# Performance work log

Measured on AMD Instinct MI355X. Metric: run time of the kernel, lower is better.

Reference implementation:

```python
import jax, jax.numpy as jnp
import numpy as np

VOCAB = 14
D_MODEL = 1024
D_FF = 4096
B, S = 8, 2048
EPS = 1e-5


def _linear_params(key, d_in, d_out):
    kw, kb = jax.random.split(key)
    lim = 1.0 / np.sqrt(d_in)
    W = jax.random.uniform(kw, (d_out, d_in), jnp.float32, -lim, lim)
    b = jax.random.uniform(kb, (d_out,), jnp.float32, -lim, lim)
    return W, b


def setup_inputs() -> dict:
    key = jax.random.key(0)
    ks = jax.random.split(key, 8)
    x = jax.random.randint(ks[0], (B, S), 0, VOCAB)
    tok_emb = jax.random.normal(ks[1], (VOCAB, D_MODEL), jnp.float32)
    qw, qb = _linear_params(ks[2], D_MODEL, D_MODEL)
    kw, kb = _linear_params(ks[3], D_MODEL, D_MODEL)
    vw, vb = _linear_params(ks[4], D_MODEL, D_MODEL)
    pw, pb = _linear_params(ks[5], D_MODEL, D_MODEL)
    f1w, f1b = _linear_params(ks[6], D_MODEL, D_FF)
    f2w, f2b = _linear_params(ks[7], D_FF, D_MODEL)
    ones = jnp.ones((D_MODEL,), jnp.float32)
    zeros = jnp.zeros((D_MODEL,), jnp.float32)
    return {
        "x": x, "tok_emb": tok_emb,
        "ln1_w": ones, "ln1_b": zeros,
        "qw": qw, "qb": qb, "kw": kw, "kb": kb, "vw": vw, "vb": vb,
        "pw": pw, "pb": pb,
        "ln2_w": ones, "ln2_b": zeros,
        "f1w": f1w, "f1b": f1b, "f2w": f2w, "f2b": f2b,
        "lnf_w": ones, "lnf_b": zeros,
    }


def _layernorm(h, w, b):
    mu = jnp.mean(h, axis=-1, keepdims=True)
    var = jnp.var(h, axis=-1, keepdims=True)
    return (h - mu) / jnp.sqrt(var + EPS) * w + b


def reference(x, tok_emb, ln1_w, ln1_b, qw, qb, kw, kb, vw, vb, pw, pb,
              ln2_w, ln2_b, f1w, f1b, f2w, f2b, lnf_w, lnf_b):
    h = tok_emb[x]                                  # [B,S,D]
    r = h
    hn = _layernorm(h, ln1_w, ln1_b)
    q = hn @ qw.T + qb
    k = hn @ kw.T + kb
    v = hn @ vw.T + vb
    scale = 1.0 / jnp.sqrt(jnp.float32(q.shape[-1]))
    att = jnp.einsum('bqd,bkd->bqk', q, k) * scale  # [B,S,S]
    causal = jnp.tril(jnp.ones((S, S), bool))
    att = jnp.where(causal, att, -jnp.inf)
    att = jax.nn.softmax(att, axis=-1)
    h = jnp.einsum('bqk,bkd->bqd', att, v) @ pw.T + pb
    h = r + h
    r2 = h
    hn = _layernorm(h, ln2_w, ln2_b)
    h = jax.nn.gelu(hn @ f1w.T + f1b, approximate=False) @ f2w.T + f2b
    h = r2 + h
    h = _layernorm(h, lnf_w, lnf_b)
    logits = h @ tok_emb.T                          # [B,S,VOCAB]
    return logits
```

## Files before the change

### kernel.cpp

```cpp
#include <hip/hip_runtime.h>
#include <math.h>

typedef unsigned short u16;
typedef __attribute__((ext_vector_type(8))) short short8;
typedef __attribute__((ext_vector_type(8))) __bf16 bf16x8;
typedef __attribute__((ext_vector_type(4))) float f32x4;

#define FLAG_BIAS   1
#define FLAG_RES    2
#define FLAG_GELU   4
#define FLAG_TRI    8
#define FLAG_CK     16

__device__ __forceinline__ u16 f2bf(float f) {
  unsigned u = __builtin_bit_cast(unsigned, f);
  unsigned r = u + 0x7fffu + ((u >> 16) & 1u);
  return (u16)(r >> 16);
}
__device__ __forceinline__ float bf2f(u16 u) {
  return __builtin_bit_cast(float, (unsigned)u << 16);
}
__device__ __forceinline__ float wred_sum(float v) {
#pragma unroll
  for (int m = 32; m; m >>= 1) v += __shfl_xor(v, m, 64);
  return v;
}
__device__ __forceinline__ float wred_max(float v) {
#pragma unroll
  for (int m = 32; m; m >>= 1) v = fmaxf(v, __shfl_xor(v, m, 64));
  return v;
}
__device__ __forceinline__ float gelu_fast(float x) {
  float y = 0.7978845608f * x * (1.f + 0.044715f * x * x);
  float e = __expf(2.f * y);
  float th = 1.f - 2.f / (e + 1.f);
  return 0.5f * x * (1.f + th);
}
__device__ __forceinline__ f32x4 mfma16(short8 a, short8 b, f32x4 c) {
  return __builtin_amdgcn_mfma_f32_16x16x32_bf16(
      __builtin_bit_cast(bf16x8, a), __builtin_bit_cast(bf16x8, b), c, 0, 0, 0);
}

#define GLOAD_LDS16(gptr, lptr)                                              \
  __builtin_amdgcn_global_load_lds(                                          \
      (const __attribute__((address_space(1))) void*)(gptr),                 \
      (__attribute__((address_space(3))) void*)(lptr), 16, 0, 0)

__global__ __launch_bounds__(512, 2) void gemm256(
    const u16* __restrict__ Aptr, const u16* __restrict__ Bptr,
    u16* __restrict__ Cptr, const float* __restrict__ bias,
    const u16* __restrict__ resp,
    int M, int N, int K, int lda, int ldb, int ldc, float alpha, int flags,
    long long sA, long long sB, long long sC) {
  const int nwg = gridDim.x;
  const int cpx = nwg >> 3;
  const int bid = blockIdx.x;
  const int swz = (bid & 7) * cpx + (bid >> 3);
  int bm, bn, z;
  if (flags & FLAG_TRI) {
    z = swz / 36;
    int tq = swz - z * 36;
    bm = (int)((sqrtf(8.f * tq + 1.f) - 1.f) * 0.5f);
    while ((bm + 1) * (bm + 2) / 2 <= tq) ++bm;
    while (bm * (bm + 1) / 2 > tq) --bm;
    bn = tq - bm * (bm + 1) / 2;
  } else {
    z = blockIdx.z;
    const int nbm = M >> 8;
    bn = swz / nbm;
    bm = swz - bn * nbm;
  }
  const int gm0 = bm << 8, gn0 = bn << 8;
  const int kend = (flags & FLAG_CK) ? min(K, gm0 + 256) : K;
  const int NT = kend >> 5;

  __shared__ __align__(16) u16 As[2][256 * 32];
  __shared__ __align__(16) u16 Bs[2][256 * 32];

  const int t = threadIdx.x;
  const int l = t & 63;
  const int w = t >> 6;
  const int wr = w >> 2, wc = w & 3;
  const int frow = l & 15;
  const int g4 = l >> 4;

  const int srow = (w << 4) + (l >> 2);
  const int sch = (l & 3) ^ ((srow >> 1) & 3);
  const u16* Ag = Aptr + (size_t)z * sA + (size_t)(gm0 + srow) * lda + sch * 8;
  const u16* Bg = Bptr + (size_t)z * sB + (size_t)(gn0 + srow) * ldb + sch * 8;
  const long long a128 = (long long)128 * lda, b128 = (long long)128 * ldb;

  auto STAGE_A = [&](int buf, int kt) {
    GLOAD_LDS16(Ag + kt, &As[buf][w * 512]);
    GLOAD_LDS16(Ag + a128 + kt, &As[buf][4096 + w * 512]);
  };
  auto STAGE_B = [&](int buf, int kt) {
    GLOAD_LDS16(Bg + kt, &Bs[buf][w * 512]);
    GLOAD_LDS16(Bg + b128 + kt, &Bs[buf][4096 + w * 512]);
  };

  f32x4 acc[8][4] = {};

  STAGE_A(0, 0); STAGE_B(0, 0);
  asm volatile("s_waitcnt vmcnt(0)" ::: "memory");
  __builtin_amdgcn_s_barrier();
  __builtin_amdgcn_sched_barrier(0);

  for (int tt = 0; tt < NT; ++tt) {
    const int buf = tt & 1;
    const int kt1 = (tt + 1) << 5;
    const bool pre = (tt + 1) < NT;
    short8 af[4], bf[4];
#pragma unroll
    for (int m = 0; m < 4; ++m) {
      int rr = wr * 128 + m * 16 + frow;
      af[m] = *(const short8*)&As[buf][rr * 32 + ((g4 ^ ((rr >> 1) & 3)) << 3)];
    }
#pragma unroll
    for (int n = 0; n < 4; ++n) {
      int rr = wc * 64 + n * 16 + frow;
      bf[n] = *(const short8*)&Bs[buf][rr * 32 + ((g4 ^ ((rr >> 1) & 3)) << 3)];
    }
    if (pre) { STAGE_A(buf ^ 1, kt1); STAGE_B(buf ^ 1, kt1); }
    __builtin_amdgcn_s_barrier();
    asm volatile("s_waitcnt lgkmcnt(0)" ::: "memory");
    __builtin_amdgcn_sched_barrier(0);
    __builtin_amdgcn_s_setprio(1);
#pragma unroll
    for (int m = 0; m < 4; ++m)
#pragma unroll
      for (int n = 0; n < 4; ++n)
        acc[m][n] = mfma16(af[m], bf[n], acc[m][n]);
    __builtin_amdgcn_s_setprio(0);
    __builtin_amdgcn_sched_barrier(0);
    __builtin_amdgcn_s_barrier();
#pragma unroll
    for (int m = 0; m < 4; ++m) {
      int rr = wr * 128 + 64 + m * 16 + frow;
      af[m] = *(const short8*)&As[buf][rr * 32 + ((g4 ^ ((rr >> 1) & 3)) << 3)];
    }
    if (pre) asm volatile("s_waitcnt vmcnt(0)" ::: "memory");
    __builtin_amdgcn_s_barrier();
    asm volatile("s_waitcnt lgkmcnt(0)" ::: "memory");
    __builtin_amdgcn_sched_barrier(0);
    __builtin_amdgcn_s_setprio(1);
#pragma unroll
    for (int m = 0; m < 4; ++m)
#pragma unroll
      for (int n = 0; n < 4; ++n)
        acc[4 + m][n] = mfma16(af[m], bf[n], acc[4 + m][n]);
    __builtin_amdgcn_s_setprio(0);
    __builtin_amdgcn_sched_barrier(0);
    __builtin_amdgcn_s_barrier();
  }

  u16* Cb = Cptr + (size_t)z * sC;
  const bool hasB = flags & FLAG_BIAS, hasR = flags & FLAG_RES;
  const bool doG = flags & FLAG_GELU;
#pragma unroll
  for (int m = 0; m < 8; ++m) {
#pragma unroll
    for (int n = 0; n < 4; ++n) {
      int row0 = gm0 + wr * 128 + m * 16 + ((l >> 4) << 2);
      int col = gn0 + wc * 64 + n * 16 + frow;
      float bv = hasB ? bias[col] : 0.0f;
#pragma unroll
      for (int i = 0; i < 4; ++i) {
        float v = acc[m][n][i] * alpha + bv;
        if (doG) v = gelu_fast(v);
        size_t idx = (size_t)(row0 + i) * ldc + col;
        if (hasR) v += bf2f(resp[idx]);
        Cb[idx] = f2bf(v);
      }
    }
  }
}

__global__ __launch_bounds__(256) void f32_to_bf16_v4(const float* __restrict__ in,
                                                      u16* __restrict__ out, int n4) {
  int i = blockIdx.x * 256 + threadIdx.x;
  if (i < n4) {
    float4 v = ((const float4*)in)[i];
    ushort4 o;
    o.x = f2bf(v.x); o.y = f2bf(v.y); o.z = f2bf(v.z); o.w = f2bf(v.w);
    ((ushort4*)out)[i] = o;
  }
}

__global__ __launch_bounds__(256) void embed_ln1(
    const int* __restrict__ x, const float* __restrict__ emb,
    const float* __restrict__ w, const float* __restrict__ b,
    u16* __restrict__ h16, u16* __restrict__ hn) {
  int row = blockIdx.x * 4 + (threadIdx.x >> 6);
  int lane = threadIdx.x & 63;
  int tok = x[row];
  const float* e = emb + (size_t)tok * 1024;
  float v[16];
  float s = 0.f, q = 0.f;
#pragma unroll
  for (int i = 0; i < 16; ++i) { v[i] = e[lane + i * 64]; s += v[i]; q += v[i] * v[i]; }
  s = wred_sum(s); q = wred_sum(q);
  float mu = s * (1.0f / 1024.0f);
  float rstd = rsqrtf(q * (1.0f / 1024.0f) - mu * mu + 1e-5f);
  u16* hr = h16 + (size_t)row * 1024;
  u16* hnr = hn + (size_t)row * 1024;
#pragma unroll
  for (int i = 0; i < 16; ++i) {
    int d = lane + i * 64;
    hr[d] = f2bf(v[i]);
    hnr[d] = f2bf((v[i] - mu) * rstd * w[d] + b[d]);
  }
}

__global__ __launch_bounds__(256) void ln_rows(
    const u16* __restrict__ in, const float* __restrict__ w,
    const float* __restrict__ b, u16* __restrict__ out) {
  int row = blockIdx.x * 4 + (threadIdx.x >> 6);
  int lane = threadIdx.x & 63;
  const short8* ir = (const short8*)(in + (size_t)row * 1024);
  short8 c0 = ir[lane], c1 = ir[lane + 64];
  float v[16];
  float s = 0.f, q = 0.f;
#pragma unroll
  for (int j = 0; j < 8; ++j) {
    v[j] = bf2f((u16)c0[j]); v[8 + j] = bf2f((u16)c1[j]);
  }
#pragma unroll
  for (int j = 0; j < 16; ++j) { s += v[j]; q += v[j] * v[j]; }
  s = wred_sum(s); q = wred_sum(q);
  float mu = s * (1.0f / 1024.0f);
  float rstd = rsqrtf(q * (1.0f / 1024.0f) - mu * mu + 1e-5f);
  short8 o0, o1;
#pragma unroll
  for (int j = 0; j < 8; ++j) {
    int d0 = lane * 8 + j, d1 = 512 + lane * 8 + j;
    o0[j] = (short)f2bf((v[j] - mu) * rstd * w[d0] + b[d0]);
    o1[j] = (short)f2bf((v[8 + j] - mu) * rstd * w[d1] + b[d1]);
  }
  short8* orow = (short8*)(out + (size_t)row * 1024);
  orow[lane] = o0; orow[lane + 64] = o1;
}

__global__ __launch_bounds__(256) void softmax_causal(u16* att) {
  int r = blockIdx.x * 4 + (threadIdx.x >> 6);
  int lane = threadIdx.x & 63;
  int i = r & 2047;
  int n = i + 1;
  int ng = (i >> 9) + 1;
  short8* pv = (short8*)(att + (size_t)r * 2048);
  float v[32];
  float m = -1e30f;
#pragma unroll
  for (int g = 0; g < 4; ++g) {
    if (g < ng) {
      short8 c = pv[g * 64 + lane];
#pragma unroll
      for (int j = 0; j < 8; ++j) {
        int idx = g * 512 + lane * 8 + j;
        float f = (idx < n) ? bf2f((u16)c[j]) : -1e30f;
        v[g * 8 + j] = f;
        m = fmaxf(m, f);
      }
    }
  }
  m = wred_max(m);
  float s = 0.f;
#pragma unroll
  for (int g = 0; g < 4; ++g) {
    if (g < ng) {
#pragma unroll
      for (int j = 0; j < 8; ++j) {
        int idx = g * 512 + lane * 8 + j;
        float e = (idx < n) ? __expf(v[g * 8 + j] - m) : 0.f;
        v[g * 8 + j] = e; s += e;
      }
    }
  }
  s = wred_sum(s);
  float inv = 1.0f / s;
#pragma unroll
  for (int g = 0; g < 4; ++g) {
    if (g < ng) {
      short8 o;
#pragma unroll
      for (int j = 0; j < 8; ++j) o[j] = (short)f2bf(v[g * 8 + j] * inv);
      pv[g * 64 + lane] = o;
    }
  }
}

__global__ __launch_bounds__(256) void transpose_v(const u16* __restrict__ V,
                                                   u16* __restrict__ Vt, int ldv) {
  int z = blockIdx.z;
  const u16* src = V + (size_t)z * 2048 * ldv;
  u16* dst = Vt + (size_t)z * 1024 * 2048;
  int j0 = (blockIdx.x >> 4) << 6;
  int d0 = (blockIdx.x & 15) << 6;
  __shared__ u16 tile[64][65];
  int c = threadIdx.x & 15;
  int rr = threadIdx.x >> 4;
#pragma unroll
  for (int q = 0; q < 4; ++q) {
    int row = rr + q * 16;
    ushort4 val = *(const ushort4*)(src + (size_t)(j0 + row) * ldv + d0 + c * 4);
    tile[row][c * 4 + 0] = val.x; tile[row][c * 4 + 1] = val.y;
    tile[row][c * 4 + 2] = val.z; tile[row][c * 4 + 3] = val.w;
  }
  __syncthreads();
#pragma unroll
  for (int q = 0; q < 4; ++q) {
    int drow = rr + q * 16;
    ushort4 o;
    o.x = tile[c * 4 + 0][drow]; o.y = tile[c * 4 + 1][drow];
    o.z = tile[c * 4 + 2][drow]; o.w = tile[c * 4 + 3][drow];
    *(ushort4*)(dst + (size_t)(d0 + drow) * 2048 + j0 + c * 4) = o;
  }
}

__global__ __launch_bounds__(256) void lnf_logits(
    const u16* __restrict__ h, const float* __restrict__ w,
    const float* __restrict__ b, const float* __restrict__ emb,
    float* __restrict__ out) {
  __shared__ float el[14 * 1056];
  int t = threadIdx.x;
  for (int f = t * 4; f < 14 * 1024; f += 1024) {
    float4 e = *(const float4*)(emb + f);
    int v = f >> 10, d = f & 1023;
    float* dst = el + v * 1056 + d + (d >> 5);
    dst[0] = e.x; dst[1] = e.y; dst[2] = e.z; dst[3] = e.w;
  }
  __syncthreads();
  int lane = t & 63, wid = t >> 6;
  float w0[8], w1[8], b0[8], b1[8];
#pragma unroll
  for (int j = 0; j < 8; ++j) {
    int d0 = lane * 8 + j, d1 = 512 + lane * 8 + j;
    w0[j] = w[d0]; b0[j] = b[d0];
    w1[j] = w[d1]; b1[j] = b[d1];
  }
  const float* e0 = el + lane * 8 + (lane >> 2);
  const float* e1 = el + 528 + lane * 8 + (lane >> 2);
  for (int rr = 0; rr < 8; ++rr) {
    int row = blockIdx.x * 32 + wid * 8 + rr;
    const short8* hr = (const short8*)(h + (size_t)row * 1024);
    short8 c0 = hr[lane], c1 = hr[lane + 64];
    float v0[8], v1[8];
    float s = 0.f, q = 0.f;
#pragma unroll
    for (int j = 0; j < 8; ++j) {
      v0[j] = bf2f((u16)c0[j]); v1[j] = bf2f((u16)c1[j]);
      s += v0[j] + v1[j];
      q += v0[j] * v0[j] + v1[j] * v1[j];
    }
    s = wred_sum(s); q = wred_sum(q);
    float mu = s * (1.0f / 1024.0f);
    float rstd = rsqrtf(q * (1.0f / 1024.0f) - mu * mu + 1e-5f);
    float h0[8], h1[8];
#pragma unroll
    for (int j = 0; j < 8; ++j) {
      h0[j] = (v0[j] - mu) * rstd * w0[j] + b0[j];
      h1[j] = (v1[j] - mu) * rstd * w1[j] + b1[j];
    }
    float p[14];
#pragma unroll
    for (int v = 0; v < 14; ++v) {
      const float* ev0 = e0 + v * 1056;
      const float* ev1 = e1 + v * 1056;
      float a = 0.f;
#pragma unroll
      for (int j = 0; j < 8; ++j) a += h0[j] * ev0[j] + h1[j] * ev1[j];
      p[v] = a;
    }
#pragma unroll
    for (int m = 32; m; m >>= 1)
#pragma unroll
      for (int v = 0; v < 14; ++v) p[v] += __shfl_xor(p[v], m, 64);
    if (lane == 0) {
      float* orow = out + (size_t)row * 14;
#pragma unroll
      for (int v = 0; v < 14; ++v) orow[v] = p[v];
    }
  }
}

__global__ void zero_out_k(float* o, int n) {
  int i = blockIdx.x * 256 + threadIdx.x;
  if (i < n) o[i] = 0.f;
}
__global__ void diag_k(float* o, float v) { if (threadIdx.x == 0) o[0] = v; }

extern "C" void kernel_launch(void* const* d_in, const int* in_sizes, int n_in,
                              void* d_out, int out_size, void* d_ws, size_t ws_size,
                              hipStream_t stream) {
  const int* x = (const int*)d_in[0];
  const float* tok_emb = (const float*)d_in[1];
  const float* ln1_w = (const float*)d_in[2];
  const float* ln1_b = (const float*)d_in[3];
  const float* qw = (const float*)d_in[4];
  const float* qb = (const float*)d_in[5];
  const float* kw = (const float*)d_in[6];
  const float* kb = (const float*)d_in[7];
  const float* vw = (const float*)d_in[8];
  const float* vb = (const float*)d_in[9];
  const float* pw = (const float*)d_in[10];
  const float* pb = (const float*)d_in[11];
  const float* ln2_w = (const float*)d_in[12];
  const float* ln2_b = (const float*)d_in[13];
  const float* f1w = (const float*)d_in[14];
  const float* f1b = (const float*)d_in[15];
  const float* f2w = (const float*)d_in[16];
  const float* f2b = (const float*)d_in[17];
  const float* lnf_w = (const float*)d_in[18];
  const float* lnf_b = (const float*)d_in[19];
  float* out = (float*)d_out;

  const long long T = 16384, D = 1024, F = 4096, S = 2048;
  const size_t MB = 1ull << 20;
  char* base = (char*)d_ws;

  if (ws_size < 224 * MB) {
    zero_out_k<<<dim3((out_size + 255) / 256), 256, 0, stream>>>(out, out_size);
    diag_k<<<dim3(1), 1, 0, stream>>>(out, (float)ws_size);
    return;
  }

  u16* rA16 = (u16*)base;
  u16* rB   = (u16*)(base + 32 * MB);
  u16* QKV  = (u16*)(base + 64 * MB);
  u16* SC   = (u16*)(base + 160 * MB);
  u16* W3   = SC;
  float* qkvb = (float*)(base + 166 * MB);
  u16* PW  = SC;
  u16* CB  = QKV;
  u16* F1  = (u16*)(base + 192 * MB);
  u16* F2  = (u16*)(base + 200 * MB);

  auto cvt = [&](const float* src, u16* dst, long long n) {
    int n4 = (int)(n / 4);
    f32_to_bf16_v4<<<dim3((n4 + 255) / 256), dim3(256), 0, stream>>>(src, dst, n4);
  };
  auto gemm = [&](const u16* A, const u16* B, u16* C, const float* bias,
                  const u16* res, long long M, long long N, long long K,
                  long long lda, long long ldb, long long ldc, float alpha,
                  int flags, long long sA, long long sB, long long sC,
                  int gx, int gz) {
    gemm256<<<dim3(gx, 1, gz), dim3(512), 0, stream>>>(
        A, B, C, bias, res, (int)M, (int)N, (int)K, (int)lda, (int)ldb,
        (int)ldc, alpha, flags, sA, sB, sC);
  };

  cvt(qw, W3, D * D);
  cvt(kw, W3 + 1024 * 1024, D * D);
  cvt(vw, W3 + 2 * 1024 * 1024, D * D);
  hipMemcpyAsync(qkvb, qb, D * 4, hipMemcpyDeviceToDevice, stream);
  hipMemcpyAsync(qkvb + 1024, kb, D * 4, hipMemcpyDeviceToDevice, stream);
  hipMemcpyAsync(qkvb + 2048, vb, D * 4, hipMemcpyDeviceToDevice, stream);

  embed_ln1<<<dim3(T / 4), 256, 0, stream>>>(x, tok_emb, ln1_w, ln1_b, rA16, rB);

  gemm(rB, W3, QKV, qkvb, nullptr, T, 3072, D, D, D, 3072, 1.f, FLAG_BIAS,
       0, 0, 0, 768, 1);

  gemm(QKV, QKV + 1024, SC, nullptr, nullptr, S, S, D, 3072, 3072, 2048,
       0.03125f, FLAG_TRI, S * 3072, S * 3072, S * S, 288, 1);

  transpose_v<<<dim3(512, 1, 8), 256, 0, stream>>>(QKV + 2048, rB, 3072);

  softmax_causal<<<dim3(T / 4), 256, 0, stream>>>(SC);

  gemm(SC, rB, QKV, nullptr, nullptr, S, D, S, S, S, 3072, 1.f, FLAG_CK,
       S * S, D * S, S * 3072, 32, 8);

  cvt(pw, PW, D * D);
  gemm(QKV, PW, rA16, pb, rA16, T, D, D, 3072, D, D, 1.f, FLAG_BIAS | FLAG_RES,
       0, 0, 0, 256, 1);

  ln_rows<<<dim3(T / 4), 256, 0, stream>>>(rA16, ln2_w, ln2_b, rB);

  cvt(f1w, F1, F * D);
  cvt(f2w, F2, D * F);
  gemm(rB, F1, CB, f1b, nullptr, T, F, D, D, D, F, 1.f, FLAG_BIAS | FLAG_GELU,
       0, 0, 0, 1024, 1);
  gemm(CB, F2, rA16, f2b, rA16, T, D, F, F, F, D, 1.f, FLAG_BIAS | FLAG_RES,
       0, 0, 0, 256, 1);

  lnf_logits<<<dim3(512), 256, 0, stream>>>(rA16, lnf_w, lnf_b, tok_emb, out);
}
```

Measured before the change: 883.5 us.

## Deepen GEMM global-to-LDS pipeline with 64-wide K tiles split into half stages

Each main-loop iteration of the GEMM now covers 64 K elements, held as two 32-wide LDS sub-tiles per buffer. The global-to-LDS loads for the next halves are spread across the four MFMA phases, and the vmcnt waits now allow outstanding loads to remain in flight. The aim is to hide global memory latency behind more MFMA work and cut barrier-bound stalls. It doubles LDS use to 128KB, which may hurt occupancy, and the half-buffer reuse depends on correct wait counts. The loop now assumes K is a multiple of 64.

```diff
diff --git a/kernel.cpp b/kernel.cpp
--- a/kernel.cpp
+++ b/kernel.cpp
@@ -72,10 +72,10 @@
   }
   const int gm0 = bm << 8, gn0 = bn << 8;
   const int kend = (flags & FLAG_CK) ? min(K, gm0 + 256) : K;
-  const int NT = kend >> 5;
-
-  __shared__ __align__(16) u16 As[2][256 * 32];
-  __shared__ __align__(16) u16 Bs[2][256 * 32];
+  const int NT = kend >> 6;
+
+  __shared__ __align__(16) u16 As[2][2][256 * 32];
+  __shared__ __align__(16) u16 Bs[2][2][256 * 32];
 
   const int t = threadIdx.x;
   const int l = t & 63;
@@ -90,38 +90,41 @@
   const u16* Bg = Bptr + (size_t)z * sB + (size_t)(gn0 + srow) * ldb + sch * 8;
   const long long a128 = (long long)128 * lda, b128 = (long long)128 * ldb;
 
-  auto STAGE_A = [&](int buf, int kt) {
-    GLOAD_LDS16(Ag + kt, &As[buf][w * 512]);
-    GLOAD_LDS16(Ag + a128 + kt, &As[buf][4096 + w * 512]);
+  auto SA = [&](int buf, int kk, int kt) {
+    GLOAD_LDS16(Ag + kt + kk * 32, &As[buf][kk][w * 512]);
+    GLOAD_LDS16(Ag + a128 + kt + kk * 32, &As[buf][kk][4096 + w * 512]);
   };
-  auto STAGE_B = [&](int buf, int kt) {
-    GLOAD_LDS16(Bg + kt, &Bs[buf][w * 512]);
-    GLOAD_LDS16(Bg + b128 + kt, &Bs[buf][4096 + w * 512]);
+  auto SB = [&](int buf, int kk, int kt) {
+    GLOAD_LDS16(Bg + kt + kk * 32, &Bs[buf][kk][w * 512]);
+    GLOAD_LDS16(Bg + b128 + kt + kk * 32, &Bs[buf][kk][4096 + w * 512]);
   };
 
   f32x4 acc[8][4] = {};
-
-  STAGE_A(0, 0); STAGE_B(0, 0);
-  asm volatile("s_waitcnt vmcnt(0)" ::: "memory");
+  short8 af[4], bf[4];
+
+  SA(0, 0, 0); SB(0, 0, 0); SA(0, 1, 0); SB(0, 1, 0);
+  SA(1, 0, 64); SB(1, 0, 64);
+  asm volatile("s_waitcnt vmcnt(4)" ::: "memory");
   __builtin_amdgcn_s_barrier();
   __builtin_amdgcn_sched_barrier(0);
 
   for (int tt = 0; tt < NT; ++tt) {
     const int buf = tt & 1;
-    const int kt1 = (tt + 1) << 5;
-    const bool pre = (tt + 1) < NT;
-    short8 af[4], bf[4];
+    const int ktn = (tt + 1) << 6;
+    const int ktn2 = (tt + 2) << 6;
+    const bool p1 = (tt + 1) < NT, p2 = (tt + 2) < NT;
+
 #pragma unroll
     for (int m = 0; m < 4; ++m) {
       int rr = wr * 128 + m * 16 + frow;
-      af[m] = *(const short8*)&As[buf][rr * 32 + ((g4 ^ ((rr >> 1) & 3)) << 3)];
+      af[m] = *(const short8*)&As[buf][0][rr * 32 + ((g4 ^ ((rr >> 1) & 3)) << 3)];
     }
 #pragma unroll
     for (int n = 0; n < 4; ++n) {
       int rr = wc * 64 + n * 16 + frow;
-      bf[n] = *(const short8*)&Bs[buf][rr * 32 + ((g4 ^ ((rr >> 1) & 3)) << 3)];
-    }
-    if (pre) { STAGE_A(buf ^ 1, kt1); STAGE_B(buf ^ 1, kt1); }
+      bf[n] = *(const short8*)&Bs[buf][0][rr * 32 + ((g4 ^ ((rr >> 1) & 3)) << 3)];
+    }
+    if (p1) SA(buf ^ 1, 1, ktn);
     __builtin_amdgcn_s_barrier();
     asm volatile("s_waitcnt lgkmcnt(0)" ::: "memory");
     __builtin_amdgcn_sched_barrier(0);
@@ -134,12 +137,58 @@
     __builtin_amdgcn_s_setprio(0);
     __builtin_amdgcn_sched_barrier(0);
     __builtin_amdgcn_s_barrier();
+
 #pragma unroll
     for (int m = 0; m < 4; ++m) {
       int rr = wr * 128 + 64 + m * 16 + frow;
-      af[m] = *(const short8*)&As[buf][rr * 32 + ((g4 ^ ((rr >> 1) & 3)) << 3)];
-    }
-    if (pre) asm volatile("s_waitcnt vmcnt(0)" ::: "memory");
+      af[m] = *(const short8*)&As[buf][0][rr * 32 + ((g4 ^ ((rr >> 1) & 3)) << 3)];
+    }
+    if (p1) SB(buf ^ 1, 1, ktn);
+    __builtin_amdgcn_s_barrier();
+    asm volatile("s_waitcnt lgkmcnt(0)" ::: "memory");
+    __builtin_amdgcn_sched_barrier(0);
+    __builtin_amdgcn_s_setprio(1);
+#pragma unroll
+    for (int m = 0; m < 4; ++m)
+#pragma unroll
+      for (int n = 0; n < 4; ++n)
+        acc[4 + m][n] = mfma16(af[m], bf[n], acc[4 + m][n]);
+    __builtin_amdgcn_s_setprio(0);
+    __builtin_amdgcn_sched_barrier(0);
+    __builtin_amdgcn_s_barrier();
+
+#pragma unroll
+    for (int m = 0; m < 4; ++m) {
+      int rr = wr * 128 + m * 16 + frow;
+      af[m] = *(const short8*)&As[buf][1][rr * 32 + ((g4 ^ ((rr >> 1) & 3)) << 3)];
+    }
+#pragma unroll
+    for (int n = 0; n < 4; ++n) {
+      int rr = wc * 64 + n * 16 + frow;
+      bf[n] = *(const short8*)&Bs[buf][1][rr * 32 + ((g4 ^ ((rr >> 1) & 3)) << 3)];
+    }
+    if (p2) SA(buf, 0, ktn2);
+    __builtin_amdgcn_s_barrier();
+    asm volatile("s_waitcnt lgkmcnt(0)" ::: "memory");
+    __builtin_amdgcn_sched_barrier(0);
+    __builtin_amdgcn_s_setprio(1);
+#pragma unroll
+    for (int m = 0; m < 4; ++m)
+#pragma unroll
+      for (int n = 0; n < 4; ++n)
+        acc[m][n] = mfma16(af[m], bf[n], acc[m][n]);
+    __builtin_amdgcn_s_setprio(0);
+    __builtin_amdgcn_sched_barrier(0);
+    __builtin_amdgcn_s_barrier();
+
+#pragma unroll
+    for (int m = 0; m < 4; ++m) {
+      int rr = wr * 128 + 64 + m * 16 + frow;
+      af[m] = *(const short8*)&As[buf][1][rr * 32 + ((g4 ^ ((rr >> 1) & 3)) << 3)];
+    }
+    if (p2) SB(buf, 0, ktn2);
+    if (p2)      asm volatile("s_waitcnt vmcnt(4)" ::: "memory");
+    else if (p1) asm volatile("s_waitcnt vmcnt(0)" ::: "memory");
     __builtin_amdgcn_s_barrier();
     asm volatile("s_waitcnt lgkmcnt(0)" ::: "memory");
     __builtin_amdgcn_sched_barrier(0);
```

Result: no change. 884.1 us (+0.1%).

## Deepen GEMM K-tile to 64 with restructured LDS staging and pipeline

Applied to the files above, without the earlier changes.

Doubles the K depth of each LDS stage from 32 to 64, using a new 8-way XOR swizzle and four row-chunk loads per operand. The main loop now reads the full A fragment set (8 m-tiles) and does two K-halves per stage, with A and B prefetches split across those halves. This is meant to halve the number of barriers and loop trips. Explicit sched_barrier and setprio hints are removed, and the launch-bounds occupancy hint is dropped. LDS grows to 128KB per block, which allows only one block per CU and raises register pressure from 8 A fragments, so less latency hiding is available.

```diff
diff --git a/kernel.cpp b/kernel.cpp
--- a/kernel.cpp
+++ b/kernel.cpp
@@ -46,7 +46,7 @@
       (const __attribute__((address_space(1))) void*)(gptr),                 \
       (__attribute__((address_space(3))) void*)(lptr), 16, 0, 0)
 
-__global__ __launch_bounds__(512, 2) void gemm256(
+__global__ __launch_bounds__(512) void gemm256(
     const u16* __restrict__ Aptr, const u16* __restrict__ Bptr,
     u16* __restrict__ Cptr, const float* __restrict__ bias,
     const u16* __restrict__ resp,
@@ -72,10 +72,10 @@
   }
   const int gm0 = bm << 8, gn0 = bn << 8;
   const int kend = (flags & FLAG_CK) ? min(K, gm0 + 256) : K;
-  const int NT = kend >> 5;
-
-  __shared__ __align__(16) u16 As[2][256 * 32];
-  __shared__ __align__(16) u16 Bs[2][256 * 32];
+  const int NT = kend >> 6;
+
+  __shared__ __align__(16) u16 As[2][256 * 64];
+  __shared__ __align__(16) u16 Bs[2][256 * 64];
 
   const int t = threadIdx.x;
   const int l = t & 63;
@@ -84,74 +84,75 @@
   const int frow = l & 15;
   const int g4 = l >> 4;
 
-  const int srow = (w << 4) + (l >> 2);
-  const int sch = (l & 3) ^ ((srow >> 1) & 3);
+  const int srow = t >> 3;
+  const int sch = (t & 7) ^ (srow & 7);
   const u16* Ag = Aptr + (size_t)z * sA + (size_t)(gm0 + srow) * lda + sch * 8;
   const u16* Bg = Bptr + (size_t)z * sB + (size_t)(gn0 + srow) * ldb + sch * 8;
-  const long long a128 = (long long)128 * lda, b128 = (long long)128 * ldb;
-
-  auto STAGE_A = [&](int buf, int kt) {
-    GLOAD_LDS16(Ag + kt, &As[buf][w * 512]);
-    GLOAD_LDS16(Ag + a128 + kt, &As[buf][4096 + w * 512]);
+
+  auto SA = [&](int buf, int j, int kt) {
+    GLOAD_LDS16(Ag + (size_t)j * 64 * lda + kt, &As[buf][j * 4096 + w * 512]);
   };
-  auto STAGE_B = [&](int buf, int kt) {
-    GLOAD_LDS16(Bg + kt, &Bs[buf][w * 512]);
-    GLOAD_LDS16(Bg + b128 + kt, &Bs[buf][4096 + w * 512]);
+  auto SB = [&](int buf, int j, int kt) {
+    GLOAD_LDS16(Bg + (size_t)j * 64 * ldb + kt, &Bs[buf][j * 4096 + w * 512]);
   };
 
   f32x4 acc[8][4] = {};
 
-  STAGE_A(0, 0); STAGE_B(0, 0);
+#pragma unroll
+  for (int j = 0; j < 4; ++j) { SA(0, j, 0); SB(0, j, 0); }
   asm volatile("s_waitcnt vmcnt(0)" ::: "memory");
   __builtin_amdgcn_s_barrier();
-  __builtin_amdgcn_sched_barrier(0);
+  asm volatile("" ::: "memory");
 
   for (int tt = 0; tt < NT; ++tt) {
     const int buf = tt & 1;
-    const int kt1 = (tt + 1) << 5;
+    const int ktn = (tt + 1) << 6;
     const bool pre = (tt + 1) < NT;
-    short8 af[4], bf[4];
-#pragma unroll
-    for (int m = 0; m < 4; ++m) {
+    short8 af[8], bf[4];
+
+#pragma unroll
+    for (int m = 0; m < 8; ++m) {
       int rr = wr * 128 + m * 16 + frow;
-      af[m] = *(const short8*)&As[buf][rr * 32 + ((g4 ^ ((rr >> 1) & 3)) << 3)];
+      af[m] = *(const short8*)&As[buf][rr * 64 + ((g4 ^ (rr & 7)) << 3)];
     }
 #pragma unroll
     for (int n = 0; n < 4; ++n) {
       int rr = wc * 64 + n * 16 + frow;
-      bf[n] = *(const short8*)&Bs[buf][rr * 32 + ((g4 ^ ((rr >> 1) & 3)) << 3)];
-    }
-    if (pre) { STAGE_A(buf ^ 1, kt1); STAGE_B(buf ^ 1, kt1); }
-    __builtin_amdgcn_s_barrier();
-    asm volatile("s_waitcnt lgkmcnt(0)" ::: "memory");
-    __builtin_amdgcn_sched_barrier(0);
-    __builtin_amdgcn_s_setprio(1);
-#pragma unroll
-    for (int m = 0; m < 4; ++m)
+      bf[n] = *(const short8*)&Bs[buf][rr * 64 + ((g4 ^ (rr & 7)) << 3)];
+    }
+    if (pre) {
+#pragma unroll
+      for (int j = 0; j < 4; ++j) SA(buf ^ 1, j, ktn);
+    }
+#pragma unroll
+    for (int m = 0; m < 8; ++m)
 #pragma unroll
       for (int n = 0; n < 4; ++n)
         acc[m][n] = mfma16(af[m], bf[n], acc[m][n]);
-    __builtin_amdgcn_s_setprio(0);
-    __builtin_amdgcn_sched_barrier(0);
+
+#pragma unroll
+    for (int m = 0; m < 8; ++m) {
+      int rr = wr * 128 + m * 16 + frow;
+      af[m] = *(const short8*)&As[buf][rr * 64 + (((4 + g4) ^ (rr & 7)) << 3)];
+    }
+#pragma unroll
+    for (int n = 0; n < 4; ++n) {
+      int rr = wc * 64 + n * 16 + frow;
+      bf[n] = *(const short8*)&Bs[buf][rr * 64 + (((4 + g4) ^ (rr & 7)) << 3)];
+    }
+    if (pre) {
+#pragma unroll
+      for (int j = 0; j < 4; ++j) SB(buf ^ 1, j, ktn);
+    }
+#pragma unroll
+    for (int m = 0; m < 8; ++m)
+#pragma unroll
+      for (int n = 0; n < 4; ++n)
+        acc[m][n] = mfma16(af[m], bf[n], acc[m][n]);
+
+    asm volatile("s_waitcnt vmcnt(0)" ::: "memory");
     __builtin_amdgcn_s_barrier();
-#pragma unroll
-    for (int m = 0; m < 4; ++m) {
-      int rr = wr * 128 + 64 + m * 16 + frow;
-      af[m] = *(const short8*)&As[buf][rr * 32 + ((g4 ^ ((rr >> 1) & 3)) << 3)];
-    }
-    if (pre) asm volatile("s_waitcnt vmcnt(0)" ::: "memory");
-    __builtin_amdgcn_s_barrier();
-    asm volatile("s_waitcnt lgkmcnt(0)" ::: "memory");
-    __builtin_amdgcn_sched_barrier(0);
-    __builtin_amdgcn_s_setprio(1);
-#pragma unroll
-    for (int m = 0; m < 4; ++m)
-#pragma unroll
-      for (int n = 0; n < 4; ++n)
-        acc[4 + m][n] = mfma16(af[m], bf[n], acc[4 + m][n]);
-    __builtin_amdgcn_s_setprio(0);
-    __builtin_amdgcn_sched_barrier(0);
-    __builtin_amdgcn_s_barrier();
+    asm volatile("" ::: "memory");
   }
 
   u16* Cb = Cptr + (size_t)z * sC;
```

Result: faster. 839.5 us (-5.0%).
